# Performance work log

Hardware: AMD Instinct MI355X
Metric: run time of the kernel (lower is better)

The kernel has to match this reference:

```python
import jax, jax.numpy as jnp
import numpy as np

B, T, C, NH = 4, 2048, 1024, 16
HD = C // NH  # head dim = 64


def setup_inputs() -> dict:
    key = jax.random.key(0)
    ks = jax.random.split(key, 5)
    s = 0.02
    return {
        "x": jax.random.normal(ks[0], (B, T, C), dtype=jnp.float32),
        "W_attn": jax.random.normal(ks[1], (C, 3 * C), dtype=jnp.float32) * s,
        "b_attn": jnp.zeros((3 * C,), dtype=jnp.float32),
        "W_proj": jax.random.normal(ks[2], (C, C), dtype=jnp.float32) * s,
        "b_proj": jnp.zeros((C,), dtype=jnp.float32),
    }


def reference(x, W_attn, b_attn, W_proj, b_proj):
    Bv, Tv, Cv = x.shape
    qkv = x @ W_attn + b_attn  # [B,T,3C]
    q, k, v = jnp.split(qkv, 3, axis=2)
    # [B,T,C] -> [B,NH,T,HD]
    def heads(t):
        return t.reshape(Bv, Tv, NH, HD).transpose(0, 2, 1, 3)
    q, k, v = heads(q), heads(k), heads(v)
    scores = jnp.einsum("bhqd,bhkd->bhqk", q, k) / jnp.sqrt(jnp.float32(HD))
    causal = jnp.tril(jnp.ones((Tv, Tv), dtype=bool))
    scores = jnp.where(causal[None, None, :, :], scores, jnp.float32(-jnp.inf))
    probs = jax.nn.softmax(scores, axis=-1)
    # dropout rate is 0.0 -> identity
    y = jnp.einsum("bhqk,bhkd->bhqd", probs, v)
    y = y.transpose(0, 2, 1, 3).reshape(Bv, Tv, Cv)
    return y @ W_proj + b_proj
```

## Files before the change

### kernel.cpp

```cpp
#include <hip/hip_runtime.h>
#include <hip/hip_bf16.h>

#define Bsz 4
#define Tseq 2048
#define Cdim 1024
#define NH 16
#define HD 64
#define Mrows (Bsz*Tseq)
#define N3C (3*Cdim)

typedef __attribute__((ext_vector_type(8))) short short8;
typedef __attribute__((ext_vector_type(4))) short short4v;
typedef __attribute__((ext_vector_type(4))) float float4v;

__device__ __forceinline__ unsigned short f2b(float f) {
    union { float f; unsigned u; } x; x.f = f;
    unsigned u = x.u;
    u += 0x7fff + ((u >> 16) & 1);
    return (unsigned short)(u >> 16);
}

__device__ __forceinline__ unsigned pk2bf(float a, float b) {
#if __has_builtin(__builtin_amdgcn_cvt_pk_bf16_f32)
    auto w = __builtin_amdgcn_cvt_pk_bf16_f32(a, b);
    unsigned u; __builtin_memcpy(&u, &w, 4);
    return u;
#else
    return (unsigned)f2b(a) | ((unsigned)f2b(b) << 16);
#endif
}

#define GLDS(gp, lp) __builtin_amdgcn_global_load_lds(                         \
    (const __attribute__((address_space(1))) unsigned*)(gp),                   \
    (__attribute__((address_space(3))) unsigned*)(lp), 16, 0, 0)

__global__ __launch_bounds__(256) void cast_kernel(const float* __restrict__ in,
                                                   unsigned short* __restrict__ out, int n) {
    int i = (blockIdx.x * 256 + threadIdx.x) * 4;
    if (i < n) {
        float4 v = *reinterpret_cast<const float4*>(in + i);
        ushort4 o;
        o.x = f2b(v.x); o.y = f2b(v.y); o.z = f2b(v.z); o.w = f2b(v.w);
        *reinterpret_cast<ushort4*>(out + i) = o;
    }
}

__global__ __launch_bounds__(256) void transpose_cast(const float* __restrict__ in,
                                                      unsigned short* __restrict__ out,
                                                      int K, int N) {
    __shared__ float tile[32][33];
    int n0 = blockIdx.x * 32, k0 = blockIdx.y * 32;
    int tx = threadIdx.x & 31, ty = threadIdx.x >> 5;
    #pragma unroll
    for (int i = 0; i < 32; i += 8)
        tile[ty + i][tx] = in[(k0 + ty + i) * N + n0 + tx];
    __syncthreads();
    #pragma unroll
    for (int i = 0; i < 32; i += 8)
        out[(size_t)(n0 + ty + i) * K + k0 + tx] = f2b(tile[tx][ty + i]);
}


#define GROW(r) ((r) * 64 + ((r) >> 3) * 8)

template<bool QKV, int NCOL>
__global__ __launch_bounds__(256) void gemm_bt(const unsigned short* __restrict__ A,
                                               const unsigned short* __restrict__ Bt,
                                               const float* __restrict__ bias,
                                               unsigned short* __restrict__ qb,
                                               unsigned short* __restrict__ kb,
                                               unsigned short* __restrict__ vb,
                                               float* __restrict__ out) {
    __shared__ unsigned short As[8320];
    __shared__ unsigned short Bs[8320];
    int tid = threadIdx.x;
    int lane = tid & 63, wave = tid >> 6;
    int wm = wave >> 1, wn = wave & 1;
    int l15 = lane & 15, quad = lane >> 4;

    int f = blockIdx.x;
    int xcd = f & 7, slot = f >> 3;
    int rowblk = xcd * 8 + (slot & 7);
    int colblk = slot >> 3;
    int row0 = rowblk * 128;
    int col0 = colblk * 128;

    const unsigned short* Ag = A + (size_t)(row0 + wave * 32 + (lane >> 3)) * Cdim + (lane & 7) * 8;
    const unsigned short* Bg = Bt + (size_t)(col0 + wave * 32 + (lane >> 3)) * Cdim + (lane & 7) * 8;
    unsigned short* Al = &As[wave * 2080];
    unsigned short* Bl = &Bs[wave * 2080];

    float4v acc[4][4] = {};

    for (int k0 = 0; k0 < Cdim; k0 += 64) {
        __syncthreads();
        #pragma unroll
        for (int c = 0; c < 4; c++) {
            GLDS(Ag + k0 + (size_t)(c * 8) * Cdim, Al + c * 520);
            GLDS(Bg + k0 + (size_t)(c * 8) * Cdim, Bl + c * 520);
        }
        __syncthreads();

        #pragma unroll
        for (int g = 0; g < 2; g++) {
            short8 af[4], bf[4];
            #pragma unroll
            for (int mi = 0; mi < 4; mi++)
                af[mi] = *(const short8*)&As[GROW(wm * 64 + mi * 16 + l15) + g * 32 + quad * 8];
            #pragma unroll
            for (int ni = 0; ni < 4; ni++)
                bf[ni] = *(const short8*)&Bs[GROW(wn * 64 + ni * 16 + l15) + g * 32 + quad * 8];
            #pragma unroll
            for (int mi = 0; mi < 4; mi++)
                #pragma unroll
                for (int ni = 0; ni < 4; ni++)
                    acc[mi][ni] = __builtin_amdgcn_mfma_f32_16x16x32_bf16(af[mi], bf[ni], acc[mi][ni], 0, 0, 0);
        }
    }

    #pragma unroll
    for (int mi = 0; mi < 4; mi++) {
        #pragma unroll
        for (int ni = 0; ni < 4; ni++) {
            int colb = col0 + wn * 64 + ni * 16 + l15;
            int rowb = row0 + wm * 64 + mi * 16 + quad * 4;
            if (QKV) {
                int p = colb >> 10;
                int h = (colb & 1023) >> 6;
                int d = colb & 63;
                int b = rowb >> 11;
                int t = rowb & 2047;
                if (p == 2) {
                    ushort4 pk;
                    pk.x = f2b(acc[mi][ni][0] + bias[colb]);
                    pk.y = f2b(acc[mi][ni][1] + bias[colb]);
                    pk.z = f2b(acc[mi][ni][2] + bias[colb]);
                    pk.w = f2b(acc[mi][ni][3] + bias[colb]);
                    *(ushort4*)&vb[((size_t)(b * NH + h) * HD + d) * Tseq + t] = pk;
                } else {
                    unsigned short* dst = (p == 0) ? qb : kb;
                    #pragma unroll
                    for (int r = 0; r < 4; r++)
                        dst[((size_t)(b * NH + h) * Tseq + (t + r)) * HD + d] =
                            f2b(acc[mi][ni][r] + bias[colb]);
                }
            } else {
                #pragma unroll
                for (int r = 0; r < 4; r++)
                    out[(size_t)(rowb + r) * Cdim + colb] = acc[mi][ni][r] + bias[colb];
            }
        }
    }
}


__global__ __launch_bounds__(256, 4) void attn_kernel(const unsigned short* __restrict__ qb,
                                                      const unsigned short* __restrict__ kb,
                                                      const unsigned short* __restrict__ vt,
                                                      unsigned short* __restrict__ yb) {
    __shared__ unsigned short Ks[2][64 * 64];
    __shared__ unsigned short Vs[2][64 * 64];

    int tid = threadIdx.x;
    int lane = tid & 63, wave = tid >> 6;
    int l15 = lane & 15, quad = lane >> 4;
    int bh = blockIdx.x;
    int qt = 15 - blockIdx.y;

    const unsigned short* Qh = qb + (size_t)bh * Tseq * HD;
    const unsigned short* Kh = kb + (size_t)bh * Tseq * HD;
    const unsigned short* Vh = vt + (size_t)bh * HD * Tseq;
    int b = bh >> 4, h = bh & 15;
    const float cexp = 0.18033688011112042f;

    int q0 = qt * 128;
    int rb0 = q0 + wave * 32;

    short8 qf[2][2];
    #pragma unroll
    for (int mi = 0; mi < 2; mi++)
        #pragma unroll
        for (int g = 0; g < 2; g++)
            qf[mi][g] = *(const short8*)(Qh + (size_t)(rb0 + mi * 16 + l15) * HD + g * 32 + quad * 8);

    int srow = lane >> 3;
    int scol = ((lane & 7) ^ srow) * 8;
    const unsigned short* Kg0 = Kh + (size_t)(wave * 16 + srow) * HD + scol;
    const unsigned short* Vg0 = Vh + (size_t)(wave * 16 + srow) * Tseq + scol;
    unsigned short* Kl0 = &Ks[0][wave * 1024];
    unsigned short* Vl0 = &Vs[0][wave * 1024];
    unsigned short* Kl1 = &Ks[1][wave * 1024];
    unsigned short* Vl1 = &Vs[1][wave * 1024];

    int sx = l15 & 7;
    int kx0 = (quad ^ sx) * 8;
    int kx1 = ((4 + quad) ^ sx) * 8;
    int qh_ = quad >> 1, ql_ = quad & 1;

    float4v ov[2][4] = {};
    float m[2]  = {-1e30f, -1e30f};
    float lp[2] = {0.f, 0.f};

    int nw = (q0 >> 6) + 2;

    GLDS(Kg0, Kl0);                GLDS(Kg0 + 8 * HD, Kl0 + 512);
    GLDS(Vg0, Vl0);                GLDS(Vg0 + 8 * Tseq, Vl0 + 512);
    __syncthreads();

    #pragma unroll 1
    for (int it = 0; it < nw; ++it) {
        int j0 = it << 6;

        if (it + 1 < nw) {
            int jn = j0 + 64;
            unsigned short* Kl = (it & 1) ? Kl0 : Kl1;
            unsigned short* Vl = (it & 1) ? Vl0 : Vl1;
            GLDS(Kg0 + (size_t)jn * HD, Kl);
            GLDS(Kg0 + (size_t)(jn + 8) * HD, Kl + 512);
            GLDS(Vg0 + jn, Vl);
            GLDS(Vg0 + 8 * Tseq + jn, Vl + 512);
        }

        if (j0 <= rb0 + 31) {
            const unsigned short* Kl = &Ks[it & 1][0];
            const unsigned short* Vl = &Vs[it & 1][0];

            float4v st[2][4];
            #pragma unroll
            for (int mi = 0; mi < 2; mi++)
                #pragma unroll
                for (int kg = 0; kg < 4; kg++)
                    st[mi][kg] = (float4v){0.f, 0.f, 0.f, 0.f};
            #pragma unroll
            for (int kg = 0; kg < 4; kg++) {
                int krow = kg * 1024 + l15 * 64;
                short8 kf0 = *(const short8*)&Kl[krow + kx0];
                short8 kf1 = *(const short8*)&Kl[krow + kx1];
                st[0][kg] = __builtin_amdgcn_mfma_f32_16x16x32_bf16(kf0, qf[0][0], st[0][kg], 0, 0, 0);
                st[0][kg] = __builtin_amdgcn_mfma_f32_16x16x32_bf16(kf1, qf[0][1], st[0][kg], 0, 0, 0);
                st[1][kg] = __builtin_amdgcn_mfma_f32_16x16x32_bf16(kf0, qf[1][0], st[1][kg], 0, 0, 0);
                st[1][kg] = __builtin_amdgcn_mfma_f32_16x16x32_bf16(kf1, qf[1][1], st[1][kg], 0, 0, 0);
            }

            if (j0 + 63 > rb0) {
                #pragma unroll
                for (int mi = 0; mi < 2; mi++) {
                    int qrow = rb0 + mi * 16 + l15;
                    #pragma unroll
                    for (int kg = 0; kg < 4; kg++) {
                        int keyb = j0 + kg * 16 + quad * 4;
                        #pragma unroll
                        for (int r = 0; r < 4; r++)
                            if (keyb + r > qrow) st[mi][kg][r] = -1e30f;
                    }
                }
            }

            short4v pf[2][4];
            #pragma unroll
            for (int mi = 0; mi < 2; mi++) {
                float mx = st[mi][0][0];
                #pragma unroll
                for (int kg = 0; kg < 4; kg++)
                    #pragma unroll
                    for (int r = 0; r < 4; r++)
                        mx = fmaxf(mx, st[mi][kg][r]);
                mx = fmaxf(mx, __shfl_xor(mx, 16));
                mx = fmaxf(mx, __shfl_xor(mx, 32));
                if (__any(mx > m[mi] + 16.0f)) {
                    float mn = fmaxf(m[mi], mx);
                    float alv = __builtin_amdgcn_exp2f((m[mi] - mn) * cexp);
                    m[mi] = mn;
                    lp[mi] *= alv;
                    float ar_[4];
                    #pragma unroll
                    for (int r = 0; r < 4; r++)
                        ar_[r] = __shfl(alv, quad * 4 + r);
                    #pragma unroll
                    for (int dg = 0; dg < 4; dg++)
                        #pragma unroll
                        for (int r = 0; r < 4; r++)
                            ov[mi][dg][r] *= ar_[r];
                }
                float mc = -m[mi] * cexp;
                float sum = 0.f;
                #pragma unroll
                for (int kg = 0; kg < 4; kg++) {
                    float p0 = __builtin_amdgcn_exp2f(__builtin_fmaf(st[mi][kg][0], cexp, mc));
                    float p1 = __builtin_amdgcn_exp2f(__builtin_fmaf(st[mi][kg][1], cexp, mc));
                    float p2 = __builtin_amdgcn_exp2f(__builtin_fmaf(st[mi][kg][2], cexp, mc));
                    float p3 = __builtin_amdgcn_exp2f(__builtin_fmaf(st[mi][kg][3], cexp, mc));
                    sum += (p0 + p1) + (p2 + p3);
                    union { unsigned u[2]; short4v s; } pk_;
                    pk_.u[0] = pk2bf(p0, p1);
                    pk_.u[1] = pk2bf(p2, p3);
                    pf[mi][kg] = pk_.s;
                }
                lp[mi] += sum;
            }

            #pragma unroll
            for (int kg = 0; kg < 4; kg++) {
                int vx = (((kg * 2 + qh_) ^ sx) << 3) + ql_ * 4;
                #pragma unroll
                for (int dg = 0; dg < 4; dg++) {
                    short4v vf = *(const short4v*)&Vl[dg * 1024 + l15 * 64 + vx];
                    ov[0][dg] = __builtin_amdgcn_mfma_f32_16x16x16bf16_1k(pf[0][kg], vf, ov[0][dg], 0, 0, 0);
                    ov[1][dg] = __builtin_amdgcn_mfma_f32_16x16x16bf16_1k(pf[1][kg], vf, ov[1][dg], 0, 0, 0);
                }
            }
        }

        __syncthreads();
    }

    #pragma unroll
    for (int mi = 0; mi < 2; mi++) {
        float lf = lp[mi];
        lf += __shfl_xor(lf, 16);
        lf += __shfl_xor(lf, 32);
        float rinv[4];
        #pragma unroll
        for (int r = 0; r < 4; r++)
            rinv[r] = 1.0f / __shfl(lf, quad * 4 + r);
        #pragma unroll
        for (int dg = 0; dg < 4; dg++)
            #pragma unroll
            for (int r = 0; r < 4; r++) {
                int t = rb0 + mi * 16 + quad * 4 + r;
                yb[((size_t)b * Tseq + t) * Cdim + h * HD + dg * 16 + l15] =
                    f2b(ov[mi][dg][r] * rinv[r]);
            }
    }
}

extern "C" void kernel_launch(void* const* d_in, const int* in_sizes, int n_in,
                              void* d_out, int out_size, void* d_ws, size_t ws_size,
                              hipStream_t stream) {
    const float* x  = (const float*)d_in[0];
    const float* Wa = (const float*)d_in[1];
    const float* ba = (const float*)d_in[2];
    const float* Wp = (const float*)d_in[3];
    const float* bp = (const float*)d_in[4];
    float* out = (float*)d_out;

    unsigned short* ws = (unsigned short*)d_ws;
    unsigned short* xb  = ws;
    unsigned short* Wat = xb  + (size_t)Mrows * Cdim;
    unsigned short* Wpt = Wat + (size_t)N3C * Cdim;
    unsigned short* qb  = Wpt + (size_t)Cdim * Cdim;
    unsigned short* kb  = qb  + (size_t)Bsz * NH * Tseq * HD;
    unsigned short* vb  = kb  + (size_t)Bsz * NH * Tseq * HD;
    unsigned short* yb  = vb  + (size_t)Bsz * NH * Tseq * HD;

    int nx = Mrows * Cdim;
    cast_kernel<<<nx / 4 / 256, 256, 0, stream>>>(x, xb, nx);
    transpose_cast<<<dim3(N3C / 32, Cdim / 32), 256, 0, stream>>>(Wa, Wat, Cdim, N3C);
    transpose_cast<<<dim3(Cdim / 32, Cdim / 32), 256, 0, stream>>>(Wp, Wpt, Cdim, Cdim);

    gemm_bt<true, 24><<<64 * 24, 256, 0, stream>>>(
        xb, Wat, ba, qb, kb, vb, nullptr);

    attn_kernel<<<dim3(Bsz * NH, 16), 256, 0, stream>>>(qb, kb, vb, yb);

    gemm_bt<false, 8><<<64 * 8, 256, 0, stream>>>(
        yb, Wpt, bp, nullptr, nullptr, nullptr, out);
}
```

Before: 266.5 us.

## Double-buffer LDS tiles in bf16 GEMM to overlap global loads with MFMA

The shared-memory A/B tiles in the GEMM kernel become two ping-pong buffers. The next K-slice is prefetched with direct global-to-LDS loads while MFMAs run on the current slice, leaving one barrier per iteration instead of two. The goal is to hide global-load latency behind matrix math. The cost is twice the LDS per block, and a launch-bounds hint of two blocks per CU is added, which may limit registers.

New measurement: 274.2 us. +2.9%, slower.

```diff
diff --git a/kernel.cpp b/kernel.cpp
--- a/kernel.cpp
+++ b/kernel.cpp
@@ -64,15 +64,15 @@
 #define GROW(r) ((r) * 64 + ((r) >> 3) * 8)
 
 template<bool QKV, int NCOL>
-__global__ __launch_bounds__(256) void gemm_bt(const unsigned short* __restrict__ A,
-                                               const unsigned short* __restrict__ Bt,
-                                               const float* __restrict__ bias,
-                                               unsigned short* __restrict__ qb,
-                                               unsigned short* __restrict__ kb,
-                                               unsigned short* __restrict__ vb,
-                                               float* __restrict__ out) {
-    __shared__ unsigned short As[8320];
-    __shared__ unsigned short Bs[8320];
+__global__ __launch_bounds__(256, 2) void gemm_bt(const unsigned short* __restrict__ A,
+                                                  const unsigned short* __restrict__ Bt,
+                                                  const float* __restrict__ bias,
+                                                  unsigned short* __restrict__ qb,
+                                                  unsigned short* __restrict__ kb,
+                                                  unsigned short* __restrict__ vb,
+                                                  float* __restrict__ out) {
+    __shared__ unsigned short As[2][8320];
+    __shared__ unsigned short Bs[2][8320];
     int tid = threadIdx.x;
     int lane = tid & 63, wave = tid >> 6;
     int wm = wave >> 1, wn = wave & 1;
@@ -87,35 +87,52 @@
 
     const unsigned short* Ag = A + (size_t)(row0 + wave * 32 + (lane >> 3)) * Cdim + (lane & 7) * 8;
     const unsigned short* Bg = Bt + (size_t)(col0 + wave * 32 + (lane >> 3)) * Cdim + (lane & 7) * 8;
-    unsigned short* Al = &As[wave * 2080];
-    unsigned short* Bl = &Bs[wave * 2080];
 
     float4v acc[4][4] = {};
 
+    {
+        unsigned short* Al = &As[0][wave * 2080];
+        unsigned short* Bl = &Bs[0][wave * 2080];
+        #pragma unroll
+        for (int c = 0; c < 4; c++) {
+            GLDS(Ag + (size_t)(c * 8) * Cdim, Al + c * 520);
+            GLDS(Bg + (size_t)(c * 8) * Cdim, Bl + c * 520);
+        }
+    }
+    __syncthreads();
+
+    int buf = 0;
     for (int k0 = 0; k0 < Cdim; k0 += 64) {
-        __syncthreads();
-        #pragma unroll
-        for (int c = 0; c < 4; c++) {
-            GLDS(Ag + k0 + (size_t)(c * 8) * Cdim, Al + c * 520);
-            GLDS(Bg + k0 + (size_t)(c * 8) * Cdim, Bl + c * 520);
-        }
-        __syncthreads();
-
+        if (k0 + 64 < Cdim) {
+            unsigned short* Al = &As[buf ^ 1][wave * 2080];
+            unsigned short* Bl = &Bs[buf ^ 1][wave * 2080];
+            #pragma unroll
+            for (int c = 0; c < 4; c++) {
+                GLDS(Ag + (k0 + 64) + (size_t)(c * 8) * Cdim, Al + c * 520);
+                GLDS(Bg + (k0 + 64) + (size_t)(c * 8) * Cdim, Bl + c * 520);
+            }
+        }
+
+        const unsigned short* Asb = &As[buf][0];
+        const unsigned short* Bsb = &Bs[buf][0];
         #pragma unroll
         for (int g = 0; g < 2; g++) {
             short8 af[4], bf[4];
             #pragma unroll
             for (int mi = 0; mi < 4; mi++)
-                af[mi] = *(const short8*)&As[GROW(wm * 64 + mi * 16 + l15) + g * 32 + quad * 8];
+                af[mi] = *(const short8*)&Asb[GROW(wm * 64 + mi * 16 + l15) + g * 32 + quad * 8];
             #pragma unroll
             for (int ni = 0; ni < 4; ni++)
-                bf[ni] = *(const short8*)&Bs[GROW(wn * 64 + ni * 16 + l15) + g * 32 + quad * 8];
+                bf[ni] = *(const short8*)&Bsb[GROW(wn * 64 + ni * 16 + l15) + g * 32 + quad * 8];
             #pragma unroll
             for (int mi = 0; mi < 4; mi++)
                 #pragma unroll
                 for (int ni = 0; ni < 4; ni++)
                     acc[mi][ni] = __builtin_amdgcn_mfma_f32_16x16x32_bf16(af[mi], bf[ni], acc[mi][ni], 0, 0, 0);
         }
+
+        __syncthreads();
+        buf ^= 1;
     }
 
     #pragma unroll
```

## Rewrite projection GEMMs with 256x128 tiles and triple-buffered LDS pipeline

Applied to the files above, without the earlier changes.

Replaces the 128x128 single-buffered GEMM with a 512-thread kernel that computes 256x128 tiles. Global-to-LDS loads are prefetched two k-steps ahead into a three-stage ring, and partial vmcnt waits replace full syncthreads. The LDS layout drops padding in favour of an XOR swizzle, and MFMA issue is raised with setprio. The goal is to hide memory latency and raise per-wave operand reuse, at the cost of much more LDS (about 144KB) and more accumulator registers, which may limit occupancy.

Measured after the change: 265.9 us. No clear change (-0.2%).

```diff
diff --git a/kernel.cpp b/kernel.cpp
--- a/kernel.cpp
+++ b/kernel.cpp
@@ -61,69 +61,93 @@
 }
 
 
-#define GROW(r) ((r) * 64 + ((r) >> 3) * 8)
-
-template<bool QKV, int NCOL>
-__global__ __launch_bounds__(256) void gemm_bt(const unsigned short* __restrict__ A,
-                                               const unsigned short* __restrict__ Bt,
-                                               const float* __restrict__ bias,
-                                               unsigned short* __restrict__ qb,
-                                               unsigned short* __restrict__ kb,
-                                               unsigned short* __restrict__ vb,
-                                               float* __restrict__ out) {
-    __shared__ unsigned short As[8320];
-    __shared__ unsigned short Bs[8320];
+template<bool QKV>
+__global__ __launch_bounds__(512, 2) void gemm256(const unsigned short* __restrict__ A,
+                                                  const unsigned short* __restrict__ Bt,
+                                                  const float* __restrict__ bias,
+                                                  unsigned short* __restrict__ qb,
+                                                  unsigned short* __restrict__ kb,
+                                                  unsigned short* __restrict__ vb,
+                                                  float* __restrict__ out) {
+    __shared__ unsigned short As[3][256 * 64];
+    __shared__ unsigned short Bs[3][128 * 64];
+
     int tid = threadIdx.x;
     int lane = tid & 63, wave = tid >> 6;
-    int wm = wave >> 1, wn = wave & 1;
+    int wm = wave >> 2, wn = wave & 3;
     int l15 = lane & 15, quad = lane >> 4;
+    int sx = l15 & 7;
 
     int f = blockIdx.x;
     int xcd = f & 7, slot = f >> 3;
-    int rowblk = xcd * 8 + (slot & 7);
-    int colblk = slot >> 3;
-    int row0 = rowblk * 128;
+    int rowblk = xcd * 4 + (slot & 3);
+    int colblk = slot >> 2;
+    int row0 = rowblk * 256;
     int col0 = colblk * 128;
 
-    const unsigned short* Ag = A + (size_t)(row0 + wave * 32 + (lane >> 3)) * Cdim + (lane & 7) * 8;
-    const unsigned short* Bg = Bt + (size_t)(col0 + wave * 32 + (lane >> 3)) * Cdim + (lane & 7) * 8;
-    unsigned short* Al = &As[wave * 2080];
-    unsigned short* Bl = &Bs[wave * 2080];
-
-    float4v acc[4][4] = {};
-
-    for (int k0 = 0; k0 < Cdim; k0 += 64) {
-        __syncthreads();
-        #pragma unroll
-        for (int c = 0; c < 4; c++) {
-            GLDS(Ag + k0 + (size_t)(c * 8) * Cdim, Al + c * 520);
-            GLDS(Bg + k0 + (size_t)(c * 8) * Cdim, Bl + c * 520);
+    int srow = lane >> 3;
+    int gsw = ((lane & 7) ^ srow) * 8;
+    const unsigned short* Ag = A + (size_t)(row0 + wave * 32 + srow) * Cdim + gsw;
+    const unsigned short* Bg = Bt + (size_t)(col0 + wave * 16 + srow) * Cdim + gsw;
+
+    float4v acc[8][2] = {};
+
+    #define STAGE256(kk, sb) do {                                              \
+        unsigned short* Al = &As[sb][wave * 32 * 64];                          \
+        unsigned short* Bl = &Bs[sb][wave * 16 * 64];                          \
+        GLDS(Ag + (kk), Al);                                                   \
+        GLDS(Ag + (kk) + (size_t)8  * Cdim, Al + 8 * 64);                      \
+        GLDS(Ag + (kk) + (size_t)16 * Cdim, Al + 16 * 64);                     \
+        GLDS(Ag + (kk) + (size_t)24 * Cdim, Al + 24 * 64);                     \
+        GLDS(Bg + (kk), Bl);                                                   \
+        GLDS(Bg + (kk) + (size_t)8  * Cdim, Bl + 8 * 64);                      \
+    } while (0)
+
+    STAGE256(0, 0);
+    STAGE256(64, 1);
+    asm volatile("s_waitcnt vmcnt(6)" ::: "memory");
+    __builtin_amdgcn_s_barrier();
+
+    int bc = 0, bp = 2;
+    #pragma unroll 1
+    for (int t = 0; t < 16; ++t) {
+        int kpre = ((t + 2) & 15) * 64;
+        STAGE256(kpre, bp);
+
+        const unsigned short* Asb = &As[bc][0];
+        const unsigned short* Bsb = &Bs[bc][0];
+        #pragma unroll
+        for (int kg = 0; kg < 2; kg++) {
+            int gcol = ((kg * 4 + quad) ^ sx) * 8;
+            short8 af[8], bf[2];
+            #pragma unroll
+            for (int mi = 0; mi < 8; mi++)
+                af[mi] = *(const short8*)&Asb[(wm * 128 + mi * 16 + l15) * 64 + gcol];
+            #pragma unroll
+            for (int ni = 0; ni < 2; ni++)
+                bf[ni] = *(const short8*)&Bsb[(wn * 32 + ni * 16 + l15) * 64 + gcol];
+            __builtin_amdgcn_s_setprio(1);
+            #pragma unroll
+            for (int mi = 0; mi < 8; mi++)
+                #pragma unroll
+                for (int ni = 0; ni < 2; ni++)
+                    acc[mi][ni] = __builtin_amdgcn_mfma_f32_16x16x32_bf16(af[mi], bf[ni], acc[mi][ni], 0, 0, 0);
+            __builtin_amdgcn_s_setprio(0);
         }
-        __syncthreads();
-
-        #pragma unroll
-        for (int g = 0; g < 2; g++) {
-            short8 af[4], bf[4];
-            #pragma unroll
-            for (int mi = 0; mi < 4; mi++)
-                af[mi] = *(const short8*)&As[GROW(wm * 64 + mi * 16 + l15) + g * 32 + quad * 8];
-            #pragma unroll
-            for (int ni = 0; ni < 4; ni++)
-                bf[ni] = *(const short8*)&Bs[GROW(wn * 64 + ni * 16 + l15) + g * 32 + quad * 8];
-            #pragma unroll
-            for (int mi = 0; mi < 4; mi++)
-                #pragma unroll
-                for (int ni = 0; ni < 4; ni++)
-                    acc[mi][ni] = __builtin_amdgcn_mfma_f32_16x16x32_bf16(af[mi], bf[ni], acc[mi][ni], 0, 0, 0);
-        }
-    }
-
-    #pragma unroll
-    for (int mi = 0; mi < 4; mi++) {
-        #pragma unroll
-        for (int ni = 0; ni < 4; ni++) {
-            int colb = col0 + wn * 64 + ni * 16 + l15;
-            int rowb = row0 + wm * 64 + mi * 16 + quad * 4;
+
+        asm volatile("s_waitcnt vmcnt(6)" ::: "memory");
+        __builtin_amdgcn_s_barrier();
+        bc = (bc == 2) ? 0 : bc + 1;
+        bp = (bp == 2) ? 0 : bp + 1;
+    }
+    #undef STAGE256
+
+    #pragma unroll
+    for (int mi = 0; mi < 8; mi++) {
+        #pragma unroll
+        for (int ni = 0; ni < 2; ni++) {
+            int colb = col0 + wn * 32 + ni * 16 + l15;
+            int rowb = row0 + wm * 128 + mi * 16 + quad * 4;
             if (QKV) {
                 int p = colb >> 10;
                 int h = (colb & 1023) >> 6;
@@ -358,11 +382,9 @@
     transpose_cast<<<dim3(N3C / 32, Cdim / 32), 256, 0, stream>>>(Wa, Wat, Cdim, N3C);
     transpose_cast<<<dim3(Cdim / 32, Cdim / 32), 256, 0, stream>>>(Wp, Wpt, Cdim, Cdim);
 
-    gemm_bt<true, 24><<<64 * 24, 256, 0, stream>>>(
-        xb, Wat, ba, qb, kb, vb, nullptr);
+    gemm256<true><<<768, 512, 0, stream>>>(xb, Wat, ba, qb, kb, vb, nullptr);
 
     attn_kernel<<<dim3(Bsz * NH, 16), 256, 0, stream>>>(qb, kb, vb, yb);
 
-    gemm_bt<false, 8><<<64 * 8, 256, 0, stream>>>(
-        yb, Wpt, bp, nullptr, nullptr, nullptr, out);
-}
+    gemm256<false><<<256, 512, 0, stream>>>(yb, Wpt, bp, nullptr, nullptr, nullptr, out);
+}
```
